# Optimization experiments

Measured on AMD Instinct MI355X. Metric: run time of the kernel, lower is better.

## Reference

```python
import jax, jax.numpy as jnp
import numpy as np

N_NODES = 50000
N_EDGES = 800000
IN_DIM = 128
HID = 64
HEADS = 4
EMB = 128
N_GRAPHS = 64
NEG_SLOPE = 0.2


def setup_inputs() -> dict:
    key = jax.random.key(0)
    ks = jax.random.split(key, 12)
    x = jax.random.normal(ks[0], (N_NODES, IN_DIM), dtype=jnp.float32)
    edge_index = jax.random.randint(ks[1], (2, N_EDGES), 0, N_NODES, dtype=jnp.int64)
    edge_weight = jax.random.uniform(ks[2], (N_EDGES,), dtype=jnp.float32)
    batch_vec = jnp.sort(jax.random.randint(ks[3], (N_NODES,), 0, N_GRAPHS, dtype=jnp.int64))
    # GATConv layer 1: in_dim -> hid, heads=4, concat
    s1 = 1.0 / np.sqrt(IN_DIM)
    W1 = jax.random.uniform(ks[4], (IN_DIM, HEADS * HID), jnp.float32, -s1, s1)
    a_src1 = jax.random.uniform(ks[5], (HEADS, HID), jnp.float32, -s1, s1)
    a_dst1 = jax.random.uniform(ks[6], (HEADS, HID), jnp.float32, -s1, s1)
    b1 = jnp.zeros((HEADS * HID,), jnp.float32)
    # GATConv layer 2: heads*hid -> emb, heads=1, mean
    s2 = 1.0 / np.sqrt(HEADS * HID)
    W2 = jax.random.uniform(ks[7], (HEADS * HID, EMB), jnp.float32, -s2, s2)
    a_src2 = jax.random.uniform(ks[8], (1, EMB), jnp.float32, -s2, s2)
    a_dst2 = jax.random.uniform(ks[9], (1, EMB), jnp.float32, -s2, s2)
    b2 = jnp.zeros((EMB,), jnp.float32)
    return {"x": x, "edge_index": edge_index, "edge_weight": edge_weight,
            "batch_vec": batch_vec, "W1": W1, "a_src1": a_src1, "a_dst1": a_dst1,
            "b1": b1, "W2": W2, "a_src2": a_src2, "a_dst2": a_dst2, "b2": b2}


def gat_conv(x, src, dst, W, a_src, a_dst, bias, heads, out_dim, concat):
    N = x.shape[0]
    h = (x @ W).reshape(N, heads, out_dim)                 # [N,H,C]
    alpha_s = jnp.sum(h * a_src, axis=-1)                  # [N,H]
    alpha_d = jnp.sum(h * a_dst, axis=-1)                  # [N,H]
    e = jax.nn.leaky_relu(alpha_s[src] + alpha_d[dst], NEG_SLOPE)  # [E,H]
    # segment softmax over edges grouped by destination node
    m = jax.ops.segment_max(e, dst, num_segments=N)        # [N,H]
    w = jnp.exp(e - m[dst])
    z = jax.ops.segment_sum(w, dst, num_segments=N)
    alpha = w / z[dst]                                     # [E,H]
    msg = h[src] * alpha[:, :, None]                       # [E,H,C]
    out = jax.ops.segment_sum(msg, dst, num_segments=N)    # [N,H,C]
    out = out.reshape(N, heads * out_dim) if concat else out.mean(axis=1)
    return out + bias


def reference(x, edge_index, edge_weight, batch_vec, W1, a_src1, a_dst1, b1, W2, a_src2, a_dst2, b2):
    N = x.shape[0]
    loop = jnp.arange(N, dtype=edge_index.dtype)
    src = jnp.concatenate([edge_index[0], loop])           # add_self_loops=True
    dst = jnp.concatenate([edge_index[1], loop])
    h = gat_conv(x, src, dst, W1, a_src1, a_dst1, b1, HEADS, HID, True)
    h = jax.nn.elu(h)                                      # dropout = identity (eval mode)
    h = gat_conv(h, src, dst, W2, a_src2, a_dst2, b2, 1, EMB, False)
    h = jax.nn.elu(h)
    # global mean pool over batch_vec
    sums = jax.ops.segment_sum(h, batch_vec, num_segments=N_GRAPHS)
    cnts = jax.ops.segment_sum(jnp.ones((N,), h.dtype), batch_vec, num_segments=N_GRAPHS)
    return sums / jnp.maximum(cnts, 1.0)[:, None]
```

## Files before the change

### kernel.cpp

```cpp
#include <hip/hip_runtime.h>
#include <hip/hip_bf16.h>
#include <cstddef>

constexpr int N_NODES = 50000;
constexpr int N_EDGES = 800000;
constexpr int IN_DIM  = 128;
constexpr int HID     = 64;
constexpr int HEADS   = 4;
constexpr int F1      = HEADS * HID;
constexpr int EMB     = 128;
constexpr int N_GRAPHS = 64;

constexpr int DEG_BLOCKS   = (N_EDGES + 255) / 256;
constexpr int SCAN_BLOCKS  = (N_NODES + 255) / 256;
constexpr int XCONV_BLOCKS = (N_NODES * IN_DIM / 4) / 256;
constexpr int W1_FRAG = 4 * 4 * 64 * 8;
constexpr int LDSB = 264;
constexpr int AXS  = HEADS * IN_DIM + 8;
constexpr int NBUCK    = (N_NODES + 255) / 256;
constexpr int P1_CHUNK = 8192;
constexpr int P1_BLOCKS = (N_EDGES + P1_CHUNK - 1) / P1_CHUNK;
constexpr int AS_BLOCKS = N_NODES / 16;
constexpr int AGG12_BLOCKS = N_NODES / 16;
static_assert(N_NODES % 16 == 0, "16-row tiling assumes exact fit");

typedef __bf16 bf16x8 __attribute__((ext_vector_type(8)));
typedef __bf16 bf16x2 __attribute__((ext_vector_type(2)));
typedef float  f32x4  __attribute__((ext_vector_type(4)));

__device__ __forceinline__ float lrelu(float x) { return x > 0.f ? x : 0.2f * x; }
__device__ __forceinline__ float eluf(float x)  { return x > 0.f ? x : expm1f(x); }

__device__ __forceinline__ void pack_frag(const float* __restrict__ B,
                                          __bf16* __restrict__ hi,
                                          __bf16* __restrict__ lo,
                                          int pblk, int NT, int KK, int ld, int col0) {
    const int gid = pblk * 256 + threadIdx.x;
    if (gid >= NT * KK * 64) return;
    const int lane = gid & 63;
    const int rem  = gid >> 6;
    const int kk   = rem % KK;
    const int t    = rem / KK;
    const int n    = col0 + t * 16 + (lane & 15);
    const int k0   = kk * 32 + (lane >> 4) * 8;
#pragma unroll
    for (int j = 0; j < 8; j++) {
        const float v = B[(size_t)(k0 + j) * ld + n];
        const __bf16 h = (__bf16)v;
        hi[(size_t)gid * 8 + j] = h;
        lo[(size_t)gid * 8 + j] = (__bf16)(v - (float)h);
    }
}

__global__ __launch_bounds__(256) void prep_kernel(const int* __restrict__ ei,
                                                   int* __restrict__ deg,
                                                   const float* __restrict__ W1,
                                                   __bf16* __restrict__ B1h,
                                                   __bf16* __restrict__ B1l,
                                                   const float* __restrict__ W2,
                                                   __bf16* __restrict__ B2h,
                                                   __bf16* __restrict__ B2l,
                                                   const float* __restrict__ as1v,
                                                   const float* __restrict__ ad1v,
                                                   float* __restrict__ wst,
                                                   const float* __restrict__ x,
                                                   __bf16* __restrict__ xb) {
    const int b = blockIdx.x;
    if (b < DEG_BLOCKS) {
        const int e = b * 256 + threadIdx.x;
        if (e < N_EDGES) atomicAdd(&deg[ei[N_EDGES + e]], 1);
        return;
    }
    const int pb = b - DEG_BLOCKS;
    if (pb < 16) {
        const int head = pb >> 2;
        pack_frag(W1, B1h + head * W1_FRAG, B1l + head * W1_FRAG,
                  pb & 3, 4, 4, F1, head * HID);
        return;
    }
    if (pb < 32) {
        pack_frag(W2, B2h, B2l, pb - 16, 8, 8, EMB, 0);
        return;
    }
    if (pb < 36) {
        const int gid = (pb - 32) * 256 + threadIdx.x;
        const int o = gid >> 7, c = gid & 127;
        const int h = o & 3;
        const float* av = (o < 4) ? as1v : ad1v;
        float s = 0.f;
#pragma unroll 8
        for (int k = 0; k < HID; k++)
            s += W1[(size_t)c * F1 + h * HID + k] * av[h * HID + k];
        wst[o * IN_DIM + c] = s;
        return;
    }
    const int i = (pb - 36) * 256 + threadIdx.x;
    const float4 v = *(const float4*)&x[(size_t)i * 4];
    __bf16 o[4] = {(__bf16)v.x, (__bf16)v.y, (__bf16)v.z, (__bf16)v.w};
    *(ulong1*)&xb[(size_t)i * 4] = *(ulong1*)o;
}

__global__ __launch_bounds__(256) void scanA_kernel(const int* __restrict__ deg,
                                                    int* __restrict__ off,
                                                    int* __restrict__ partial, int N) {
    __shared__ int sm[256];
    const int t = threadIdx.x;
    const int i = blockIdx.x * 256 + t;
    const int v = (i < N) ? deg[i] : 0;
    sm[t] = v;
    __syncthreads();
    int val = v;
#pragma unroll
    for (int o = 1; o < 256; o <<= 1) {
        const int add = (t >= o) ? sm[t - o] : 0;
        __syncthreads();
        val += add;
        sm[t] = val;
        __syncthreads();
    }
    if (i < N) off[i] = val - v;
    if (t == 255) partial[blockIdx.x] = val;
}

__global__ __launch_bounds__(256) void scanB_kernel(int* __restrict__ partial,
                                                    int* __restrict__ off_last) {
    __shared__ int sm[256];
    const int t = threadIdx.x;
    const int v = (t < SCAN_BLOCKS) ? partial[t] : 0;
    sm[t] = v;
    __syncthreads();
    int val = v;
#pragma unroll
    for (int o = 1; o < 256; o <<= 1) {
        const int add = (t >= o) ? sm[t - o] : 0;
        __syncthreads();
        val += add;
        sm[t] = val;
        __syncthreads();
    }
    if (t < SCAN_BLOCKS) partial[t] = val - v;
    if (t == SCAN_BLOCKS - 1) *off_last = val;
}

__global__ __launch_bounds__(256) void scanC_kernel(int* __restrict__ off,
                                                    const int* __restrict__ partial,
                                                    int* __restrict__ cur,
                                                    int* __restrict__ gcur, int N) {
    const int i = blockIdx.x * 256 + threadIdx.x;
    if (i < N) {
        const int o = off[i] + partial[blockIdx.x];
        off[i] = o;
        cur[i] = 0;
        if ((i & 255) == 0) gcur[i >> 8] = o;
    }
}

__global__ __launch_bounds__(256) void as_scatter_kernel(
        const float* __restrict__ x, const float* __restrict__ wst,
        float* __restrict__ as_out, float* __restrict__ ad_out,
        const int* __restrict__ ei, int* __restrict__ gcur,
        unsigned* __restrict__ stage) {
    const int tid = threadIdx.x;
    if (blockIdx.x < AS_BLOCKS) {
        const int n   = blockIdx.x * 16 + (tid >> 4);
        const int l16 = tid & 15;
        const int d8  = l16 * 8;
        const float4 xa = *(const float4*)&x[(size_t)n * IN_DIM + d8];
        const float4 xc = *(const float4*)&x[(size_t)n * IN_DIM + d8 + 4];
        float p[8];
#pragma unroll
        for (int o = 0; o < 8; o++) {
            const float4 wa = *(const float4*)&wst[o * IN_DIM + d8];
            const float4 wb = *(const float4*)&wst[o * IN_DIM + d8 + 4];
            p[o] = xa.x * wa.x + xa.y * wa.y + xa.z * wa.z + xa.w * wa.w
                 + xc.x * wb.x + xc.y * wb.y + xc.z * wb.z + xc.w * wb.w;
        }
#pragma unroll
        for (int off = 1; off < 16; off <<= 1) {
#pragma unroll
            for (int o = 0; o < 8; o++) p[o] += __shfl_xor(p[o], off);
        }
        if (l16 == 0) {
            *(float4*)&as_out[n * HEADS] = (float4){p[0], p[1], p[2], p[3]};
            *(float4*)&ad_out[n * HEADS] = (float4){p[4], p[5], p[6], p[7]};
        }
        return;
    }
    __shared__ int lhist[NBUCK];
    __shared__ int lbase[NBUCK];
    const int e0 = (blockIdx.x - AS_BLOCKS) * P1_CHUNK;
    for (int b = tid; b < NBUCK; b += 256) lhist[b] = 0;
    __syncthreads();
    for (int i = 0; i < P1_CHUNK / 256; i++) {
        const int e = e0 + i * 256 + tid;
        if (e < N_EDGES) atomicAdd(&lhist[ei[N_EDGES + e] >> 8], 1);
    }
    __syncthreads();
    for (int b = tid; b < NBUCK; b += 256) {
        const int c = lhist[b];
        lbase[b] = c ? atomicAdd(&gcur[b], c) : 0;
    }
    __syncthreads();
    for (int b = tid; b < NBUCK; b += 256) lhist[b] = 0;
    __syncthreads();
    for (int i = 0; i < P1_CHUNK / 256; i++) {
        const int e = e0 + i * 256 + tid;
        if (e < N_EDGES) {
            const int s = ei[e], d = ei[N_EDGES + e];
            const int bk = d >> 8;
            const int r  = atomicAdd(&lhist[bk], 1);
            stage[lbase[bk] + r] = (unsigned)s | ((unsigned)d << 16);
        }
    }
}

__global__ __launch_bounds__(256) void w1s_kernel(const unsigned* __restrict__ stage,
                                                  const int* __restrict__ off,
                                                  int* __restrict__ cur,
                                                  const float* __restrict__ as1,
                                                  const float* __restrict__ ad1,
                                                  int* __restrict__ col,
                                                  float4* __restrict__ w4, int E) {
    const int i = blockIdx.x * 256 + threadIdx.x;
    if (i >= E) return;
    const unsigned p = stage[i];
    const int s = (int)(p & 0xFFFFu);
    const int d = (int)(p >> 16);
    const float4 a = *(const float4*)&as1[s * HEADS];
    const float4 b = *(const float4*)&ad1[d * HEADS];
    const int pos = off[d] + atomicAdd(&cur[d], 1);
    float4 o;
    o.x = expf(lrelu(a.x + b.x));
    o.y = expf(lrelu(a.y + b.y));
    o.z = expf(lrelu(a.z + b.z));
    o.w = expf(lrelu(a.w + b.w));
    col[pos] = s;
    w4[pos] = o;
}

__global__ __launch_bounds__(256, 4) void agg_gemm12_kernel(
        const int* __restrict__ off, const int* __restrict__ col,
        const float4* __restrict__ w4, const __bf16* __restrict__ xb,
        const float* __restrict__ as1, const float* __restrict__ ad1,
        const __bf16* __restrict__ B1h, const __bf16* __restrict__ B1l,
        const float* __restrict__ b1,
        const __bf16* __restrict__ B2h, const __bf16* __restrict__ B2l,
        const float* __restrict__ avs, const float* __restrict__ avd,
        __bf16* __restrict__ g2b, float* __restrict__ as_out,
        float* __restrict__ ad_out, int M) {
    __shared__ __bf16 axh[16 * AXS];
    __shared__ __bf16 axl[16 * AXS];
    __shared__ float pps[4][16], pdd[4][16];
    __bf16* const smh = axh;
    __bf16* const sml = axl;
    const int tid  = threadIdx.x;
    const int wave = tid >> 6, lane = tid & 63;
    const int quad = lane >> 4, l16 = lane & 15;
    const int row0 = blockIdx.x * 16;

    {
        const int ln = wave * 4 + quad;
        const int w  = row0 + ln;
        const int d8 = l16 * 8;
        float acc[HEADS][8];
        float z[HEADS];
        {
            const float4 asv = *(const float4*)&as1[w * HEADS];
            const float4 adv = *(const float4*)&ad1[w * HEADS];
            const float ws0 = expf(lrelu(asv.x + adv.x));
            const float ws1 = expf(lrelu(asv.y + adv.y));
            const float ws2 = expf(lrelu(asv.z + adv.z));
            const float ws3 = expf(lrelu(asv.w + adv.w));
            const bf16x8 xv = *(const bf16x8*)&xb[(size_t)w * IN_DIM + d8];
#pragma unroll
            for (int d = 0; d < 8; d++) {
                const float xf = (float)xv[d];
                acc[0][d] = ws0 * xf; acc[1][d] = ws1 * xf;
                acc[2][d] = ws2 * xf; acc[3][d] = ws3 * xf;
            }
            z[0] = ws0; z[1] = ws1; z[2] = ws2; z[3] = ws3;
        }
        const int jb = off[w], je = off[w + 1];
        int j = jb;
        for (; j + 3 < je; j += 4) {
            int    s[4];
            float4 ww[4];
            bf16x8 bv[4];
#pragma unroll
            for (int u = 0; u < 4; u++) s[u] = col[j + u];
#pragma unroll
            for (int u = 0; u < 4; u++) ww[u] = w4[j + u];
#pragma unroll
            for (int u = 0; u < 4; u++)
                bv[u] = *(const bf16x8*)&xb[(size_t)s[u] * IN_DIM + d8];
#pragma unroll
            for (int u = 0; u < 4; u++) {
#pragma unroll
                for (int d = 0; d < 8; d++) {
                    const float xf = (float)bv[u][d];
                    acc[0][d] += ww[u].x * xf;
                    acc[1][d] += ww[u].y * xf;
                    acc[2][d] += ww[u].z * xf;
                    acc[3][d] += ww[u].w * xf;
                }
                z[0] += ww[u].x; z[1] += ww[u].y;
                z[2] += ww[u].z; z[3] += ww[u].w;
            }
        }
        for (; j < je; j++) {
            const int s0 = col[j];
            const float4 w0 = w4[j];
            const bf16x8 b0 = *(const bf16x8*)&xb[(size_t)s0 * IN_DIM + d8];
#pragma unroll
            for (int d = 0; d < 8; d++) {
                const float xf = (float)b0[d];
                acc[0][d] += w0.x * xf; acc[1][d] += w0.y * xf;
                acc[2][d] += w0.z * xf; acc[3][d] += w0.w * xf;
            }
            z[0] += w0.x; z[1] += w0.y; z[2] += w0.z; z[3] += w0.w;
        }
#pragma unroll
        for (int h = 0; h < HEADS; h++) {
            const float inv = 1.f / z[h];
            bf16x8 hv, lv;
#pragma unroll
            for (int d = 0; d < 8; d++) {
                const float v = acc[h][d] * inv;
                const __bf16 hh = (__bf16)v;
                hv[d] = hh;
                lv[d] = (__bf16)(v - (float)hh);
            }
            const int o = ln * AXS + h * IN_DIM + d8;
            *(bf16x8*)&axh[o] = hv;
            *(bf16x8*)&axl[o] = lv;
        }
    }
    __syncthreads();

    {
        bf16x8 ahv[4], alv[4];
        const int abase = l16 * AXS + wave * IN_DIM;
#pragma unroll
        for (int kk = 0; kk < 4; kk++) {
            const int k0 = kk * 32 + quad * 8;
            ahv[kk] = *(const bf16x8*)&axh[abase + k0];
            alv[kk] = *(const bf16x8*)&axl[abase + k0];
        }
        __syncthreads();

        f32x4 acc1[4];
#pragma unroll
        for (int t = 0; t < 4; t++) acc1[t] = (f32x4){0.f, 0.f, 0.f, 0.f};
#pragma unroll
        for (int kk = 0; kk < 4; kk++) {
#pragma unroll
            for (int t = 0; t < 4; t++) {
                const size_t bi = (size_t)wave * W1_FRAG +
                                  ((size_t)(t * 4 + kk) * 64 + lane) * 8;
                bf16x8 bhv = *(const bf16x8*)&B1h[bi];
                bf16x8 blv = *(const bf16x8*)&B1l[bi];
                acc1[t] = __builtin_amdgcn_mfma_f32_16x16x32_bf16(ahv[kk], bhv, acc1[t], 0, 0, 0);
                acc1[t] = __builtin_amdgcn_mfma_f32_16x16x32_bf16(alv[kk], bhv, acc1[t], 0, 0, 0);
                acc1[t] = __builtin_amdgcn_mfma_f32_16x16x32_bf16(ahv[kk], blv, acc1[t], 0, 0, 0);
            }
        }
#pragma unroll
        for (int t = 0; t < 4; t++) {
            const int c = wave * 64 + t * 16 + l16;
            const float bb = b1[c];
#pragma unroll
            for (int r = 0; r < 4; r++) {
                const float v = eluf(acc1[t][r] + bb);
                const __bf16 hh = (__bf16)v;
                smh[(quad * 4 + r) * LDSB + c] = hh;
                sml[(quad * 4 + r) * LDSB + c] = (__bf16)(v - (float)hh);
            }
        }
    }
    __syncthreads();

    f32x4 acc2[2];
#pragma unroll
    for (int t = 0; t < 2; t++) acc2[t] = (f32x4){0.f, 0.f, 0.f, 0.f};
    const int arow = l16 * LDSB;
#pragma unroll
    for (int kk = 0; kk < 8; kk++) {
        const int k0 = kk * 32 + quad * 8;
        bf16x8 ah = *(const bf16x8*)&smh[arow + k0];
        bf16x8 al = *(const bf16x8*)&sml[arow + k0];
#pragma unroll
        for (int tt = 0; tt < 2; tt++) {
            const int t = wave * 2 + tt;
            const size_t bi = ((size_t)(t * 8 + kk) * 64 + lane) * 8;
            bf16x8 bhv = *(const bf16x8*)&B2h[bi];
            bf16x8 blv = *(const bf16x8*)&B2l[bi];
            acc2[tt] = __builtin_amdgcn_mfma_f32_16x16x32_bf16(ah, bhv, acc2[tt], 0, 0, 0);
            acc2[tt] = __builtin_amdgcn_mfma_f32_16x16x32_bf16(al, bhv, acc2[tt], 0, 0, 0);
            acc2[tt] = __builtin_amdgcn_mfma_f32_16x16x32_bf16(ah, blv, acc2[tt], 0, 0, 0);
        }
    }

    const int rowS = row0 + quad * 4;
#pragma unroll
    for (int tt = 0; tt < 2; tt++) {
        const int t = wave * 2 + tt;
#pragma unroll
        for (int r = 0; r < 4; r++) {
            const int rr = rowS + r;
            if (rr < M) g2b[(size_t)rr * EMB + t * 16 + l16] = (__bf16)acc2[tt][r];
        }
    }
#pragma unroll
    for (int r = 0; r < 4; r++) {
        float ps = 0.f, pd = 0.f;
#pragma unroll
        for (int tt = 0; tt < 2; tt++) {
            const int c = (wave * 2 + tt) * 16 + l16;
            ps += acc2[tt][r] * avs[c];
            pd += acc2[tt][r] * avd[c];
        }
#pragma unroll
        for (int o = 1; o < 16; o <<= 1) {
            ps += __shfl_xor(ps, o);
            pd += __shfl_xor(pd, o);
        }
        if (l16 == 0) {
            pps[wave][quad * 4 + r] = ps;
            pdd[wave][quad * 4 + r] = pd;
        }
    }
    __syncthreads();
    if (tid < 16) {
        const int rr = row0 + tid;
        if (rr < M) {
            as_out[rr] = pps[0][tid] + pps[1][tid] + pps[2][tid] + pps[3][tid];
            ad_out[rr] = pdd[0][tid] + pdd[1][tid] + pdd[2][tid] + pdd[3][tid];
        }
    }
}

__global__ __launch_bounds__(256) void agg2_kernel(const int* __restrict__ off,
                                                   const int* __restrict__ col,
                                                   const float* __restrict__ as2,
                                                   const float* __restrict__ ad2,
                                                   const __bf16* __restrict__ g2b,
                                                   float* __restrict__ out2, int N) {
    const int w = __builtin_amdgcn_readfirstlane((blockIdx.x * 256 + threadIdx.x) >> 6);
    const int lane = threadIdx.x & 63;
    if (w >= N) return;

    const float ad2w = ad2[w];
    float2 acc = make_float2(0.f, 0.f);
    float z = 0.f;
    {
        const float wt = expf(lrelu(as2[w] + ad2w));
        const bf16x2 hv = *(const bf16x2*)&g2b[(size_t)w * EMB + lane * 2];
        acc.x += wt * (float)hv[0]; acc.y += wt * (float)hv[1];
        z += wt;
    }
    const int jb = off[w], je = off[w + 1];
    int j = jb;
    for (; j + 3 < je; j += 4) {
        const int s0 = col[j], s1 = col[j + 1], s2 = col[j + 2], s3 = col[j + 3];
        const float w0 = expf(lrelu(as2[s0] + ad2w));
        const float w1 = expf(lrelu(as2[s1] + ad2w));
        const float w2v = expf(lrelu(as2[s2] + ad2w));
        const float w3 = expf(lrelu(as2[s3] + ad2w));
        const bf16x2 b0 = *(const bf16x2*)&g2b[(size_t)s0 * EMB + lane * 2];
        const bf16x2 b1 = *(const bf16x2*)&g2b[(size_t)s1 * EMB + lane * 2];
        const bf16x2 b2 = *(const bf16x2*)&g2b[(size_t)s2 * EMB + lane * 2];
        const bf16x2 b3 = *(const bf16x2*)&g2b[(size_t)s3 * EMB + lane * 2];
        acc.x += w0 * (float)b0[0] + w1 * (float)b1[0] + w2v * (float)b2[0] + w3 * (float)b3[0];
        acc.y += w0 * (float)b0[1] + w1 * (float)b1[1] + w2v * (float)b2[1] + w3 * (float)b3[1];
        z += (w0 + w1) + (w2v + w3);
    }
    for (; j < je; j++) {
        const int s0 = col[j];
        const float w0 = expf(lrelu(as2[s0] + ad2w));
        const bf16x2 b0 = *(const bf16x2*)&g2b[(size_t)s0 * EMB + lane * 2];
        acc.x += w0 * (float)b0[0]; acc.y += w0 * (float)b0[1];
        z += w0;
    }
    const float inv = 1.f / z;
    float2 o = make_float2(acc.x * inv, acc.y * inv);
    *(float2*)&out2[(size_t)w * EMB + lane * 2] = o;
}

__global__ __launch_bounds__(128) void pool_kernel(const float* __restrict__ out2,
                                                   const float* __restrict__ b2,
                                                   const int* __restrict__ batch,
                                                   float* __restrict__ pool,
                                                   float* __restrict__ cnt, int N) {
    const int c = threadIdx.x;
    const int n0 = blockIdx.x * 64;
    const int nend = min(n0 + 64, N);
    const float bias = b2[c];
    float acc = 0.f, cacc = 0.f;
    int curg = batch[n0];
    for (int n = n0; n < nend; n++) {
        const int g = batch[n];
        if (g != curg) {
            atomicAdd(&pool[curg * EMB + c], acc);
            if (c == 0) atomicAdd(&cnt[curg], cacc);
            acc = 0.f; cacc = 0.f; curg = g;
        }
        float v = out2[(size_t)n * EMB + c] + bias;
        v = v > 0.f ? v : expm1f(v);
        acc += v;
        cacc += 1.f;
    }
    atomicAdd(&pool[curg * EMB + c], acc);
    if (c == 0) atomicAdd(&cnt[curg], cacc);
}

__global__ __launch_bounds__(256) void div_kernel(const float* __restrict__ pool,
                                                  const float* __restrict__ cnt,
                                                  float* __restrict__ out) {
    const int i = blockIdx.x * 256 + threadIdx.x;
    out[i] = pool[i] / fmaxf(cnt[i >> 7], 1.f);
}

extern "C" void kernel_launch(void* const* d_in, const int* in_sizes, int n_in,
                              void* d_out, int out_size, void* d_ws, size_t ws_size,
                              hipStream_t stream) {
    const float* x      = (const float*)d_in[0];
    const int*   ei     = (const int*)d_in[1];
    const int*   batch  = (const int*)d_in[3];
    const float* W1     = (const float*)d_in[4];
    const float* a_src1 = (const float*)d_in[5];
    const float* a_dst1 = (const float*)d_in[6];
    const float* b1     = (const float*)d_in[7];
    const float* W2     = (const float*)d_in[8];
    const float* a_src2 = (const float*)d_in[9];
    const float* a_dst2 = (const float*)d_in[10];
    const float* b2     = (const float*)d_in[11];
    float* out = (float*)d_out;

    const int N = N_NODES, E = N_EDGES;

    size_t cur_off = 0;
    auto carve = [&](size_t bytes) {
        size_t o = cur_off;
        cur_off = (cur_off + bytes + 255) & ~(size_t)255;
        return (char*)d_ws + o;
    };
    int* deg     = (int*)carve((size_t)N * 4);
    float* pool  = (float*)carve((size_t)N_GRAPHS * EMB * 4);
    float* cnt   = (float*)carve((size_t)N_GRAPHS * 4);
    const size_t zero_bytes = cur_off;
    int* curp    = (int*)carve((size_t)N * 4);
    int* partial = (int*)carve((size_t)SCAN_BLOCKS * 4);
    int* gcur    = (int*)carve((size_t)NBUCK * 4);
    unsigned* stage = (unsigned*)carve((size_t)E * 4);
    float* wst   = (float*)carve((size_t)8 * IN_DIM * 4);
    __bf16* B1h  = (__bf16*)carve((size_t)HEADS * W1_FRAG * 2);
    __bf16* B1l  = (__bf16*)carve((size_t)HEADS * W1_FRAG * 2);
    __bf16* B2h  = (__bf16*)carve((size_t)F1 * EMB * 2);
    __bf16* B2l  = (__bf16*)carve((size_t)F1 * EMB * 2);
    __bf16* xb   = (__bf16*)carve((size_t)N * IN_DIM * 2);
    int* off     = (int*)carve((size_t)(N + 1) * 4);
    int* col     = (int*)carve((size_t)E * 4);
    float4* w4   = (float4*)carve((size_t)E * 16);
    __bf16* g2b  = (__bf16*)carve((size_t)N * EMB * 2);
    float* out2  = (float*)carve((size_t)N * EMB * 4);
    float* as1   = (float*)carve((size_t)N * HEADS * 4);
    float* ad1   = (float*)carve((size_t)N * HEADS * 4);
    float* as2   = (float*)carve((size_t)N * 4);
    float* ad2   = (float*)carve((size_t)N * 4);

    hipMemsetAsync(d_ws, 0, zero_bytes, stream);

    prep_kernel<<<DEG_BLOCKS + 36 + XCONV_BLOCKS, 256, 0, stream>>>(
        ei, deg, W1, B1h, B1l, W2, B2h, B2l, a_src1, a_dst1, wst, x, xb);

    scanA_kernel<<<SCAN_BLOCKS, 256, 0, stream>>>(deg, off, partial, N);
    scanB_kernel<<<1, 256, 0, stream>>>(partial, &off[N]);
    scanC_kernel<<<SCAN_BLOCKS, 256, 0, stream>>>(off, partial, curp, gcur, N);

    as_scatter_kernel<<<AS_BLOCKS + P1_BLOCKS, 256, 0, stream>>>(
        x, wst, as1, ad1, ei, gcur, stage);

    w1s_kernel<<<DEG_BLOCKS, 256, 0, stream>>>(stage, off, curp, as1, ad1, col, w4, E);

    agg_gemm12_kernel<<<AGG12_BLOCKS, 256, 0, stream>>>(off, col, w4, xb, as1, ad1,
                                                        B1h, B1l, b1, B2h, B2l,
                                                        a_src2, a_dst2,
                                                        g2b, as2, ad2, N);

    agg2_kernel<<<(N + 3) / 4, 256, 0, stream>>>(off, col, as2, ad2, g2b, out2, N);

    pool_kernel<<<(N + 63) / 64, 128, 0, stream>>>(out2, b2, batch, pool, cnt, N);
    div_kernel<<<(N_GRAPHS * EMB) / 256, 256, 0, stream>>>(pool, cnt, out);
}
```

Baseline: 337.0 us.

## Aggregate layer-1 neighbor features with MFMA over edge chunks and use fast exp

Replaces the per-row scalar FMA aggregation in the fused layer-1 kernel with a block-level scheme. The block stages 32 neighbor feature rows at a time transposed and swizzled into LDS, builds a masked bf16 hi/lo attention-weight matrix, and accumulates with 16x16x32 bf16 MFMAs, adding a final self-loop chunk. It also swaps expf for __expf in the weight computations. The MFMA path spends matrix work on masked zeros and adds two barriers per chunk, and the split bf16 weights plus fast exp slightly change precision.

```diff
diff --git a/kernel.cpp b/kernel.cpp
--- a/kernel.cpp
+++ b/kernel.cpp
@@ -17,6 +17,7 @@
 constexpr int W1_FRAG = 4 * 4 * 64 * 8;
 constexpr int LDSB = 264;
 constexpr int AXS  = HEADS * IN_DIM + 8;
+constexpr int ESTR = 40;
 constexpr int NBUCK    = (N_NODES + 255) / 256;
 constexpr int P1_CHUNK = 8192;
 constexpr int P1_BLOCKS = (N_EDGES + P1_CHUNK - 1) / P1_CHUNK;
@@ -230,10 +231,10 @@
     const float4 b = *(const float4*)&ad1[d * HEADS];
     const int pos = off[d] + atomicAdd(&cur[d], 1);
     float4 o;
-    o.x = expf(lrelu(a.x + b.x));
-    o.y = expf(lrelu(a.y + b.y));
-    o.z = expf(lrelu(a.z + b.z));
-    o.w = expf(lrelu(a.w + b.w));
+    o.x = __expf(lrelu(a.x + b.x));
+    o.y = __expf(lrelu(a.y + b.y));
+    o.z = __expf(lrelu(a.z + b.z));
+    o.w = __expf(lrelu(a.w + b.w));
     col[pos] = s;
     w4[pos] = o;
 }
@@ -248,9 +249,13 @@
         const float* __restrict__ avs, const float* __restrict__ avd,
         __bf16* __restrict__ g2b, float* __restrict__ as_out,
         float* __restrict__ ad_out, int M) {
-    __shared__ __bf16 axh[16 * AXS];
-    __shared__ __bf16 axl[16 * AXS];
+    __shared__ __align__(16) __bf16 uni[2 * 16 * AXS];
+    __shared__ float alpha_s[HEADS * 32];
+    __shared__ int   offs[17];
     __shared__ float pps[4][16], pdd[4][16];
+    __bf16* const axh = uni;
+    __bf16* const axl = uni + 16 * AXS;
+    __bf16* const XTR = uni;
     __bf16* const smh = axh;
     __bf16* const sml = axl;
     const int tid  = threadIdx.x;
@@ -258,81 +263,95 @@
     const int quad = lane >> 4, l16 = lane & 15;
     const int row0 = blockIdx.x * 16;
 
+    if (tid < 17) offs[tid] = off[row0 + tid];
     {
-        const int ln = wave * 4 + quad;
-        const int w  = row0 + ln;
-        const int d8 = l16 * 8;
-        float acc[HEADS][8];
-        float z[HEADS];
-        {
-            const float4 asv = *(const float4*)&as1[w * HEADS];
-            const float4 adv = *(const float4*)&ad1[w * HEADS];
-            const float ws0 = expf(lrelu(asv.x + adv.x));
-            const float ws1 = expf(lrelu(asv.y + adv.y));
-            const float ws2 = expf(lrelu(asv.z + adv.z));
-            const float ws3 = expf(lrelu(asv.w + adv.w));
-            const bf16x8 xv = *(const bf16x8*)&xb[(size_t)w * IN_DIM + d8];
-#pragma unroll
-            for (int d = 0; d < 8; d++) {
-                const float xf = (float)xv[d];
-                acc[0][d] = ws0 * xf; acc[1][d] = ws1 * xf;
-                acc[2][d] = ws2 * xf; acc[3][d] = ws3 * xf;
+        unsigned* z4 = (unsigned*)XTR;
+        for (int i = tid; i < 128 * ESTR / 2; i += 256) z4[i] = 0u;
+    }
+    __syncthreads();
+    const int ebase0 = offs[0], eend = offs[16];
+    const int nreal  = (eend - ebase0 + 31) >> 5;
+    const int off_n  = offs[l16], off_n1 = offs[l16 + 1];
+
+    f32x4 acc[8];
+#pragma unroll
+    for (int t = 0; t < 8; t++) acc[t] = (f32x4){0.f, 0.f, 0.f, 0.f};
+    float zacc = 0.f;
+
+    for (int c = 0; c <= nreal; c++) {
+        const bool is_self = (c == nreal);
+        const int ebase = ebase0 + c * 32;
+#pragma unroll
+        for (int g = 0; g < 2; g++) {
+            const int r = wave * 8 + g * 4 + quad;
+            int srcn = -1;
+            if (is_self) { if (r < 16) srcn = row0 + r; }
+            else          srcn = col[min(ebase + r, N_EDGES - 1)];
+            if (srcn >= 0) {
+                const bf16x8 xv = *(const bf16x8*)&xb[(size_t)srcn * IN_DIM + l16 * 8];
+                const int swz = (l16 & 3) << 3;
+                const int slot = r ^ swz;
+#pragma unroll
+                for (int dd = 0; dd < 8; dd++)
+                    XTR[(l16 * 8 + dd) * ESTR + slot] = xv[dd];
             }
-            z[0] = ws0; z[1] = ws1; z[2] = ws2; z[3] = ws3;
-        }
-        const int jb = off[w], je = off[w + 1];
-        int j = jb;
-        for (; j + 3 < je; j += 4) {
-            int    s[4];
-            float4 ww[4];
-            bf16x8 bv[4];
-#pragma unroll
-            for (int u = 0; u < 4; u++) s[u] = col[j + u];
-#pragma unroll
-            for (int u = 0; u < 4; u++) ww[u] = w4[j + u];
-#pragma unroll
-            for (int u = 0; u < 4; u++)
-                bv[u] = *(const bf16x8*)&xb[(size_t)s[u] * IN_DIM + d8];
-#pragma unroll
-            for (int u = 0; u < 4; u++) {
-#pragma unroll
-                for (int d = 0; d < 8; d++) {
-                    const float xf = (float)bv[u][d];
-                    acc[0][d] += ww[u].x * xf;
-                    acc[1][d] += ww[u].y * xf;
-                    acc[2][d] += ww[u].z * xf;
-                    acc[3][d] += ww[u].w * xf;
-                }
-                z[0] += ww[u].x; z[1] += ww[u].y;
-                z[2] += ww[u].z; z[3] += ww[u].w;
+        }
+        if (lane < 32) {
+            float av;
+            if (is_self)
+                av = (lane < 16)
+                   ? __expf(lrelu(as1[(row0 + lane) * HEADS + wave] +
+                                  ad1[(row0 + lane) * HEADS + wave]))
+                   : 0.f;
+            else
+                av = ((const float*)w4)[(size_t)min(ebase + lane, N_EDGES - 1) * 4 + wave];
+            alpha_s[wave * 32 + lane] = av;
+        }
+        __syncthreads();
+
+        float av8[8];
+        *(float4*)&av8[0] = *(const float4*)&alpha_s[wave * 32 + quad * 8];
+        *(float4*)&av8[4] = *(const float4*)&alpha_s[wave * 32 + quad * 8 + 4];
+        bf16x8 bh, bl;
+#pragma unroll
+        for (int j = 0; j < 8; j++) {
+            const int k = quad * 8 + j;
+            bool in;
+            if (is_self) in = (k == l16);
+            else { const int e = ebase + k; in = (e >= off_n) && (e < off_n1); }
+            const float a = in ? av8[j] : 0.f;
+            zacc += a;
+            const __bf16 h = (__bf16)a;
+            bh[j] = h;
+            bl[j] = (__bf16)(a - (float)h);
+        }
+#pragma unroll
+        for (int t = 0; t < 8; t++) {
+            const int dim = t * 16 + l16;
+            const int k0  = (quad * 8) ^ (((dim >> 3) & 3) << 3);
+            const bf16x8 af = *(const bf16x8*)&XTR[dim * ESTR + k0];
+            acc[t] = __builtin_amdgcn_mfma_f32_16x16x32_bf16(af, bh, acc[t], 0, 0, 0);
+            acc[t] = __builtin_amdgcn_mfma_f32_16x16x32_bf16(af, bl, acc[t], 0, 0, 0);
+        }
+        __syncthreads();
+    }
+
+    zacc += __shfl_xor(zacc, 16);
+    zacc += __shfl_xor(zacc, 32);
+    const float inv = 1.f / zacc;
+
+    {
+#pragma unroll
+        for (int t = 0; t < 8; t++) {
+#pragma unroll
+            for (int rp = 0; rp < 4; rp += 2) {
+                const float v0 = acc[t][rp] * inv, v1 = acc[t][rp + 1] * inv;
+                const __bf16 h0 = (__bf16)v0, h1 = (__bf16)v1;
+                const int o = l16 * AXS + wave * IN_DIM + t * 16 + quad * 4 + rp;
+                *(bf16x2*)&axh[o] = (bf16x2){h0, h1};
+                *(bf16x2*)&axl[o] = (bf16x2){(__bf16)(v0 - (float)h0),
+                                             (__bf16)(v1 - (float)h1)};
             }
-        }
-        for (; j < je; j++) {
-            const int s0 = col[j];
-            const float4 w0 = w4[j];
-            const bf16x8 b0 = *(const bf16x8*)&xb[(size_t)s0 * IN_DIM + d8];
-#pragma unroll
-            for (int d = 0; d < 8; d++) {
-                const float xf = (float)b0[d];
-                acc[0][d] += w0.x * xf; acc[1][d] += w0.y * xf;
-                acc[2][d] += w0.z * xf; acc[3][d] += w0.w * xf;
-            }
-            z[0] += w0.x; z[1] += w0.y; z[2] += w0.z; z[3] += w0.w;
-        }
-#pragma unroll
-        for (int h = 0; h < HEADS; h++) {
-            const float inv = 1.f / z[h];
-            bf16x8 hv, lv;
-#pragma unroll
-            for (int d = 0; d < 8; d++) {
-                const float v = acc[h][d] * inv;
-                const __bf16 hh = (__bf16)v;
-                hv[d] = hh;
-                lv[d] = (__bf16)(v - (float)hh);
-            }
-            const int o = ln * AXS + h * IN_DIM + d8;
-            *(bf16x8*)&axh[o] = hv;
-            *(bf16x8*)&axl[o] = lv;
         }
     }
     __syncthreads();
@@ -453,7 +472,7 @@
     float2 acc = make_float2(0.f, 0.f);
     float z = 0.f;
     {
-        const float wt = expf(lrelu(as2[w] + ad2w));
+        const float wt = __expf(lrelu(as2[w] + ad2w));
         const bf16x2 hv = *(const bf16x2*)&g2b[(size_t)w * EMB + lane * 2];
         acc.x += wt * (float)hv[0]; acc.y += wt * (float)hv[1];
         z += wt;
@@ -462,10 +481,10 @@
     int j = jb;
     for (; j + 3 < je; j += 4) {
         const int s0 = col[j], s1 = col[j + 1], s2 = col[j + 2], s3 = col[j + 3];
-        const float w0 = expf(lrelu(as2[s0] + ad2w));
-        const float w1 = expf(lrelu(as2[s1] + ad2w));
-        const float w2v = expf(lrelu(as2[s2] + ad2w));
-        const float w3 = expf(lrelu(as2[s3] + ad2w));
+        const float w0 = __expf(lrelu(as2[s0] + ad2w));
+        const float w1 = __expf(lrelu(as2[s1] + ad2w));
+        const float w2v = __expf(lrelu(as2[s2] + ad2w));
+        const float w3 = __expf(lrelu(as2[s3] + ad2w));
         const bf16x2 b0 = *(const bf16x2*)&g2b[(size_t)s0 * EMB + lane * 2];
         const bf16x2 b1 = *(const bf16x2*)&g2b[(size_t)s1 * EMB + lane * 2];
         const bf16x2 b2 = *(const bf16x2*)&g2b[(size_t)s2 * EMB + lane * 2];
@@ -476,7 +495,7 @@
     }
     for (; j < je; j++) {
         const int s0 = col[j];
-        const float w0 = expf(lrelu(as2[s0] + ad2w));
+        const float w0 = __expf(lrelu(as2[s0] + ad2w));
         const bf16x2 b0 = *(const bf16x2*)&g2b[(size_t)s0 * EMB + lane * 2];
         acc.x += w0 * (float)b0[0]; acc.y += w0 * (float)b0[1];
         z += w0;
```

After: 375.1 us. +11.3%, slower.

## Remap layer-2 aggregation to 16 lanes per node and use fast exp

Applied to the files above, without the earlier changes.

The layer-2 aggregation kernel now handles 16 nodes per block with 16 lanes per node, each lane loading 8 bf16 features at once instead of 64 lanes each loading 2. Neighbor indices, attention scores and feature rows are batched four at a time to overlap the gathers, and the output is written as float4 pairs. Separately, expf is replaced by the __expf intrinsic in the attention-weight computations of three kernels. The aim is wider, fewer memory transactions per gathered row, more nodes per wave, and cheaper exponentials, at the cost of slightly lower exp accuracy and more registers per thread.

```diff
diff --git a/kernel.cpp b/kernel.cpp
--- a/kernel.cpp
+++ b/kernel.cpp
@@ -230,10 +230,10 @@
     const float4 b = *(const float4*)&ad1[d * HEADS];
     const int pos = off[d] + atomicAdd(&cur[d], 1);
     float4 o;
-    o.x = expf(lrelu(a.x + b.x));
-    o.y = expf(lrelu(a.y + b.y));
-    o.z = expf(lrelu(a.z + b.z));
-    o.w = expf(lrelu(a.w + b.w));
+    o.x = __expf(lrelu(a.x + b.x));
+    o.y = __expf(lrelu(a.y + b.y));
+    o.z = __expf(lrelu(a.z + b.z));
+    o.w = __expf(lrelu(a.w + b.w));
     col[pos] = s;
     w4[pos] = o;
 }
@@ -267,10 +267,10 @@
         {
             const float4 asv = *(const float4*)&as1[w * HEADS];
             const float4 adv = *(const float4*)&ad1[w * HEADS];
-            const float ws0 = expf(lrelu(asv.x + adv.x));
-            const float ws1 = expf(lrelu(asv.y + adv.y));
-            const float ws2 = expf(lrelu(asv.z + adv.z));
-            const float ws3 = expf(lrelu(asv.w + adv.w));
+            const float ws0 = __expf(lrelu(asv.x + adv.x));
+            const float ws1 = __expf(lrelu(asv.y + adv.y));
+            const float ws2 = __expf(lrelu(asv.z + adv.z));
+            const float ws3 = __expf(lrelu(asv.w + adv.w));
             const bf16x8 xv = *(const bf16x8*)&xb[(size_t)w * IN_DIM + d8];
 #pragma unroll
             for (int d = 0; d < 8; d++) {
@@ -445,45 +445,53 @@
                                                    const float* __restrict__ ad2,
                                                    const __bf16* __restrict__ g2b,
                                                    float* __restrict__ out2, int N) {
-    const int w = __builtin_amdgcn_readfirstlane((blockIdx.x * 256 + threadIdx.x) >> 6);
-    const int lane = threadIdx.x & 63;
-    if (w >= N) return;
-
+    const int w  = blockIdx.x * 16 + (threadIdx.x >> 4);
+    const int d8 = (threadIdx.x & 15) * 8;
     const float ad2w = ad2[w];
-    float2 acc = make_float2(0.f, 0.f);
-    float z = 0.f;
+    float acc[8];
+    float z;
     {
-        const float wt = expf(lrelu(as2[w] + ad2w));
-        const bf16x2 hv = *(const bf16x2*)&g2b[(size_t)w * EMB + lane * 2];
-        acc.x += wt * (float)hv[0]; acc.y += wt * (float)hv[1];
-        z += wt;
+        const float wt = __expf(lrelu(as2[w] + ad2w));
+        const bf16x8 hv = *(const bf16x8*)&g2b[(size_t)w * EMB + d8];
+#pragma unroll
+        for (int d = 0; d < 8; d++) acc[d] = wt * (float)hv[d];
+        z = wt;
     }
     const int jb = off[w], je = off[w + 1];
     int j = jb;
     for (; j + 3 < je; j += 4) {
-        const int s0 = col[j], s1 = col[j + 1], s2 = col[j + 2], s3 = col[j + 3];
-        const float w0 = expf(lrelu(as2[s0] + ad2w));
-        const float w1 = expf(lrelu(as2[s1] + ad2w));
-        const float w2v = expf(lrelu(as2[s2] + ad2w));
-        const float w3 = expf(lrelu(as2[s3] + ad2w));
-        const bf16x2 b0 = *(const bf16x2*)&g2b[(size_t)s0 * EMB + lane * 2];
-        const bf16x2 b1 = *(const bf16x2*)&g2b[(size_t)s1 * EMB + lane * 2];
-        const bf16x2 b2 = *(const bf16x2*)&g2b[(size_t)s2 * EMB + lane * 2];
-        const bf16x2 b3 = *(const bf16x2*)&g2b[(size_t)s3 * EMB + lane * 2];
-        acc.x += w0 * (float)b0[0] + w1 * (float)b1[0] + w2v * (float)b2[0] + w3 * (float)b3[0];
-        acc.y += w0 * (float)b0[1] + w1 * (float)b1[1] + w2v * (float)b2[1] + w3 * (float)b3[1];
-        z += (w0 + w1) + (w2v + w3);
+        int s[4];
+#pragma unroll
+        for (int u = 0; u < 4; u++) s[u] = col[j + u];
+        float av[4];
+#pragma unroll
+        for (int u = 0; u < 4; u++) av[u] = as2[s[u]];
+        bf16x8 bv[4];
+#pragma unroll
+        for (int u = 0; u < 4; u++)
+            bv[u] = *(const bf16x8*)&g2b[(size_t)s[u] * EMB + d8];
+#pragma unroll
+        for (int u = 0; u < 4; u++) {
+            const float wt = __expf(lrelu(av[u] + ad2w));
+#pragma unroll
+            for (int d = 0; d < 8; d++) acc[d] += wt * (float)bv[u][d];
+            z += wt;
+        }
     }
     for (; j < je; j++) {
         const int s0 = col[j];
-        const float w0 = expf(lrelu(as2[s0] + ad2w));
-        const bf16x2 b0 = *(const bf16x2*)&g2b[(size_t)s0 * EMB + lane * 2];
-        acc.x += w0 * (float)b0[0]; acc.y += w0 * (float)b0[1];
-        z += w0;
+        const float wt = __expf(lrelu(as2[s0] + ad2w));
+        const bf16x8 b0 = *(const bf16x8*)&g2b[(size_t)s0 * EMB + d8];
+#pragma unroll
+        for (int d = 0; d < 8; d++) acc[d] += wt * (float)b0[d];
+        z += wt;
     }
     const float inv = 1.f / z;
-    float2 o = make_float2(acc.x * inv, acc.y * inv);
-    *(float2*)&out2[(size_t)w * EMB + lane * 2] = o;
+    float4 o0, o1;
+    o0.x = acc[0] * inv; o0.y = acc[1] * inv; o0.z = acc[2] * inv; o0.w = acc[3] * inv;
+    o1.x = acc[4] * inv; o1.y = acc[5] * inv; o1.z = acc[6] * inv; o1.w = acc[7] * inv;
+    *(float4*)&out2[(size_t)w * EMB + d8]     = o0;
+    *(float4*)&out2[(size_t)w * EMB + d8 + 4] = o1;
 }
 
 __global__ __launch_bounds__(128) void pool_kernel(const float* __restrict__ out2,
@@ -587,7 +595,7 @@
                                                         a_src2, a_dst2,
                                                         g2b, as2, ad2, N);
 
-    agg2_kernel<<<(N + 3) / 4, 256, 0, stream>>>(off, col, as2, ad2, g2b, out2, N);
+    agg2_kernel<<<AGG12_BLOCKS, 256, 0, stream>>>(off, col, as2, ad2, g2b, out2, N);
 
     pool_kernel<<<(N + 63) / 64, 128, 0, stream>>>(out2, b2, batch, pool, cnt, N);
     div_kernel<<<(N_GRAPHS * EMB) / 256, 256, 0, stream>>>(pool, cnt, out);
```

Result: faster. 329.3 us (-2.3%).
